# Kernel tuning notes

Measured on AMD Instinct MI355X. Metric: run time of the kernel, lower is better.

Reference implementation:

```python
import jax, jax.numpy as jnp
import numpy as np
from jax import lax

T = 32768
INPUT = 1024
HIDDEN = 1024
OUTPUT = 1024


def setup_inputs() -> dict:
    key = jax.random.key(0)
    k1, k2, k3, k4, k5 = jax.random.split(key, 5)
    return {
        "x": jax.random.normal(k1, (1, T, INPUT), dtype=jnp.float32),
        "W_i2h": jax.random.normal(k2, (HIDDEN, INPUT + HIDDEN), dtype=jnp.float32) * 0.02,
        "b_i2h": jax.random.normal(k3, (HIDDEN,), dtype=jnp.float32) * 0.02,
        "W_h2o": jax.random.normal(k4, (OUTPUT, HIDDEN), dtype=jnp.float32) * 0.02,
        "b_h2o": jax.random.normal(k5, (OUTPUT,), dtype=jnp.float32) * 0.02,
    }


def reference(x, W_i2h, b_i2h, W_h2o, b_h2o):
    # x: [1, T, input]; original iterates timesteps of x[0] with batch-1 state.
    seq = x[0]  # [T, input]
    h0 = jnp.zeros((1, HIDDEN), dtype=x.dtype)

    # Split i2h weight so we avoid a per-step concat: [hidden, input+hidden]
    W_x = W_i2h[:, :INPUT]   # acts on token
    W_h = W_i2h[:, INPUT:]   # acts on hidden

    def step(h, x_t):
        # h: [1, hidden], x_t: [input]
        h_new = jnp.tanh(x_t[None, :] @ W_x.T + h @ W_h.T + b_i2h)
        return h_new, None

    h_T, _ = lax.scan(step, h0, seq)
    # Original computes h2o every step but returns only the last output.
    output = h_T @ W_h2o.T + b_h2o  # [1, output]
    return output
```

## Files before the change

kernel.cpp:

```cpp
#include <hip/hip_runtime.h>

#define T_STEPS 32768
#define HID 1024
#define NWG 64
#define RPG 16

__device__ __forceinline__ unsigned short f2bf(float f) {
    unsigned u = __float_as_uint(f);
    u = (u + 0x7fffu + ((u >> 16) & 1u)) >> 16;
    return (unsigned short)u;
}
__device__ __forceinline__ float bf2f(unsigned short s) {
    return __uint_as_float(((unsigned)s) << 16);
}

#define BM 64
#define BN 64
#define BK 16
#define LDST 68

__global__ void __launch_bounds__(256) pre_gemm(
    const float* __restrict__ x, const float* __restrict__ Wi,
    const float* __restrict__ b, unsigned short* __restrict__ pre)
{
    __shared__ float As[BK * LDST];
    __shared__ float Bs[BK * LDST];
    const int tid = threadIdx.x;
    const int t0 = blockIdx.x * BM;
    const int j0 = blockIdx.y * BN;
    const int row = tid >> 2;
    const int kq  = tid & 3;
    const int tx  = tid & 15;
    const int ty  = tid >> 4;

    float c[4][4];
#pragma unroll
    for (int i = 0; i < 4; ++i)
#pragma unroll
        for (int j = 0; j < 4; ++j) c[i][j] = 0.f;

    for (int k0 = 0; k0 < 1024; k0 += BK) {
        float4 a4 = *(const float4*)&x[(size_t)(t0 + row) * 1024 + k0 + 4 * kq];
        float4 b4 = *(const float4*)&Wi[(size_t)(j0 + row) * 2048 + k0 + 4 * kq];
        __syncthreads();
        As[(4 * kq + 0) * LDST + row] = a4.x;
        As[(4 * kq + 1) * LDST + row] = a4.y;
        As[(4 * kq + 2) * LDST + row] = a4.z;
        As[(4 * kq + 3) * LDST + row] = a4.w;
        Bs[(4 * kq + 0) * LDST + row] = b4.x;
        Bs[(4 * kq + 1) * LDST + row] = b4.y;
        Bs[(4 * kq + 2) * LDST + row] = b4.z;
        Bs[(4 * kq + 3) * LDST + row] = b4.w;
        __syncthreads();
#pragma unroll
        for (int kk = 0; kk < BK; ++kk) {
            float4 av = *(const float4*)&As[kk * LDST + 4 * ty];
            float4 bv = *(const float4*)&Bs[kk * LDST + 4 * tx];
            c[0][0] = fmaf(av.x, bv.x, c[0][0]); c[0][1] = fmaf(av.x, bv.y, c[0][1]);
            c[0][2] = fmaf(av.x, bv.z, c[0][2]); c[0][3] = fmaf(av.x, bv.w, c[0][3]);
            c[1][0] = fmaf(av.y, bv.x, c[1][0]); c[1][1] = fmaf(av.y, bv.y, c[1][1]);
            c[1][2] = fmaf(av.y, bv.z, c[1][2]); c[1][3] = fmaf(av.y, bv.w, c[1][3]);
            c[2][0] = fmaf(av.z, bv.x, c[2][0]); c[2][1] = fmaf(av.z, bv.y, c[2][1]);
            c[2][2] = fmaf(av.z, bv.z, c[2][2]); c[2][3] = fmaf(av.z, bv.w, c[2][3]);
            c[3][0] = fmaf(av.w, bv.x, c[3][0]); c[3][1] = fmaf(av.w, bv.y, c[3][1]);
            c[3][2] = fmaf(av.w, bv.z, c[3][2]); c[3][3] = fmaf(av.w, bv.w, c[3][3]);
        }
    }

    float4 bias = *(const float4*)&b[j0 + 4 * tx];
#pragma unroll
    for (int i = 0; i < 4; ++i) {
        int r = t0 + 4 * ty + i;
        ushort4 u;
        u.x = f2bf(c[i][0] + bias.x);
        u.y = f2bf(c[i][1] + bias.y);
        u.z = f2bf(c[i][2] + bias.z);
        u.w = f2bf(c[i][3] + bias.w);
        *(ushort4*)&pre[(size_t)r * 1024 + j0 + 4 * tx] = u;
    }
}


__device__ __forceinline__ unsigned long long pack_hv(float v, unsigned t) {
    return ((unsigned long long)t << 32) | (unsigned long long)__float_as_uint(v);
}

__device__ __forceinline__ void poll_stage(unsigned long long* src, float* dst,
                                           unsigned tg, int e0)
{
    unsigned long long p0, p1, p2, p3;
    for (;;) {
        p0 = __hip_atomic_load(&src[e0 + 0], __ATOMIC_RELAXED, __HIP_MEMORY_SCOPE_AGENT);
        p1 = __hip_atomic_load(&src[e0 + 1], __ATOMIC_RELAXED, __HIP_MEMORY_SCOPE_AGENT);
        p2 = __hip_atomic_load(&src[e0 + 2], __ATOMIC_RELAXED, __HIP_MEMORY_SCOPE_AGENT);
        p3 = __hip_atomic_load(&src[e0 + 3], __ATOMIC_RELAXED, __HIP_MEMORY_SCOPE_AGENT);
        if ((unsigned)(p0 >> 32) == tg && (unsigned)(p1 >> 32) == tg &&
            (unsigned)(p2 >> 32) == tg && (unsigned)(p3 >> 32) == tg) break;
    }
    dst[e0 + 0] = __uint_as_float((unsigned)p0);
    dst[e0 + 1] = __uint_as_float((unsigned)p1);
    dst[e0 + 2] = __uint_as_float((unsigned)p2);
    dst[e0 + 3] = __uint_as_float((unsigned)p3);
}

__device__ __forceinline__ float wave_sum(float v) {
#pragma unroll
    for (int off = 32; off > 0; off >>= 1) v += __shfl_xor(v, off, 64);
    return v;
}

__global__ void __launch_bounds__(256) rnn_rec(
    const unsigned short* __restrict__ pre,
    const float* __restrict__ Wi,
    const float* __restrict__ Wo,
    const float* __restrict__ bo,
    float* __restrict__ out,
    unsigned long long* hp)
{
    const int g   = blockIdx.x;
    const int tid = threadIdx.x;
    const int w   = tid >> 6;
    const int l   = tid & 63;
    const int rowbase = g * RPG + w * 4;
    const int e0 = tid * 4;

    __shared__ float hl[2][HID];

    float4 wv[4][4];
#pragma unroll
    for (int rr = 0; rr < 4; ++rr)
#pragma unroll
        for (int j = 0; j < 4; ++j)
            wv[rr][j] = *(const float4*)&Wi[(size_t)(rowbase + rr) * 2048 + 1024 + 4 * l + 256 * j];

    if (tid < RPG)
        __hip_atomic_store(&hp[g * RPG + tid], pack_hv(0.f, 0u),
                           __ATOMIC_RELAXED, __HIP_MEMORY_SCOPE_AGENT);

    for (int t = 1; t <= T_STEPS; ++t) {
        float prev = 0.f;
        if (l < 4) prev = bf2f(pre[(size_t)(t - 1) * HID + rowbase + l]);

        unsigned long long* src = &hp[((t - 1) & 1) * HID];
        float* dst = hl[(t - 1) & 1];
        poll_stage(src, dst, (unsigned)(t - 1), e0);
        __syncthreads();

        float s0 = 0.f, s1 = 0.f, s2 = 0.f, s3 = 0.f;
#pragma unroll
        for (int j = 0; j < 4; ++j) {
            float4 hv = *(const float4*)&dst[4 * l + 256 * j];
            s0 = fmaf(wv[0][j].x, hv.x, s0); s0 = fmaf(wv[0][j].y, hv.y, s0);
            s0 = fmaf(wv[0][j].z, hv.z, s0); s0 = fmaf(wv[0][j].w, hv.w, s0);
            s1 = fmaf(wv[1][j].x, hv.x, s1); s1 = fmaf(wv[1][j].y, hv.y, s1);
            s1 = fmaf(wv[1][j].z, hv.z, s1); s1 = fmaf(wv[1][j].w, hv.w, s1);
            s2 = fmaf(wv[2][j].x, hv.x, s2); s2 = fmaf(wv[2][j].y, hv.y, s2);
            s2 = fmaf(wv[2][j].z, hv.z, s2); s2 = fmaf(wv[2][j].w, hv.w, s2);
            s3 = fmaf(wv[3][j].x, hv.x, s3); s3 = fmaf(wv[3][j].y, hv.y, s3);
            s3 = fmaf(wv[3][j].z, hv.z, s3); s3 = fmaf(wv[3][j].w, hv.w, s3);
        }
        s0 = wave_sum(s0); s1 = wave_sum(s1); s2 = wave_sum(s2); s3 = wave_sum(s3);

        if (l < 4) {
            float sv = (l == 0) ? s0 : (l == 1) ? s1 : (l == 2) ? s2 : s3;
            float h = tanhf(prev + sv);
            __hip_atomic_store(&hp[(t & 1) * HID + rowbase + l], pack_hv(h, (unsigned)t),
                               __ATOMIC_RELAXED, __HIP_MEMORY_SCOPE_AGENT);
        }
    }

    {
        unsigned long long* src = &hp[(T_STEPS & 1) * HID];
        float* dst = hl[0];
        poll_stage(src, dst, (unsigned)T_STEPS, e0);
        __syncthreads();

        float s0 = 0.f, s1 = 0.f, s2 = 0.f, s3 = 0.f;
#pragma unroll
        for (int j = 0; j < 4; ++j) {
            float4 hv = *(const float4*)&dst[4 * l + 256 * j];
            float4 w0 = *(const float4*)&Wo[(size_t)(rowbase + 0) * 1024 + 4 * l + 256 * j];
            float4 w1 = *(const float4*)&Wo[(size_t)(rowbase + 1) * 1024 + 4 * l + 256 * j];
            float4 w2 = *(const float4*)&Wo[(size_t)(rowbase + 2) * 1024 + 4 * l + 256 * j];
            float4 w3 = *(const float4*)&Wo[(size_t)(rowbase + 3) * 1024 + 4 * l + 256 * j];
            s0 = fmaf(w0.x, hv.x, s0); s0 = fmaf(w0.y, hv.y, s0);
            s0 = fmaf(w0.z, hv.z, s0); s0 = fmaf(w0.w, hv.w, s0);
            s1 = fmaf(w1.x, hv.x, s1); s1 = fmaf(w1.y, hv.y, s1);
            s1 = fmaf(w1.z, hv.z, s1); s1 = fmaf(w1.w, hv.w, s1);
            s2 = fmaf(w2.x, hv.x, s2); s2 = fmaf(w2.y, hv.y, s2);
            s2 = fmaf(w2.z, hv.z, s2); s2 = fmaf(w2.w, hv.w, s2);
            s3 = fmaf(w3.x, hv.x, s3); s3 = fmaf(w3.y, hv.y, s3);
            s3 = fmaf(w3.z, hv.z, s3); s3 = fmaf(w3.w, hv.w, s3);
        }
        s0 = wave_sum(s0); s1 = wave_sum(s1); s2 = wave_sum(s2); s3 = wave_sum(s3);
        if (l < 4) {
            float sv = (l == 0) ? s0 : (l == 1) ? s1 : (l == 2) ? s2 : s3;
            out[rowbase + l] = sv + bo[rowbase + l];
        }
    }
}

extern "C" void kernel_launch(void* const* d_in, const int* in_sizes, int n_in,
                              void* d_out, int out_size, void* d_ws, size_t ws_size,
                              hipStream_t stream) {
    const float* x     = (const float*)d_in[0];
    const float* W_i2h = (const float*)d_in[1];
    const float* b_i2h = (const float*)d_in[2];
    const float* W_h2o = (const float*)d_in[3];
    const float* b_h2o = (const float*)d_in[4];
    float* out = (float*)d_out;

    unsigned short* pre = (unsigned short*)d_ws;
    unsigned long long* hp =
        (unsigned long long*)((char*)d_ws + (size_t)T_STEPS * HID * sizeof(unsigned short));

    pre_gemm<<<dim3(T_STEPS / BM, HID / BN), 256, 0, stream>>>(x, W_i2h, b_i2h, pre);
    rnn_rec<<<NWG, 256, 0, stream>>>(pre, W_i2h, W_h2o, b_h2o, out, hp);
}
```

Baseline: 57.47 ms.

## Rework recurrent kernel polling, row mapping, staged pre loads and fast tanh

Rewrites the persistent recurrence kernel. Each 16-lane group now owns one hidden row, reduced with a short 4-step shuffle. Hidden-state polling uses inline-asm double-buffered sc1 loads with a spin budget, and stores go out with sc1 as well. Precomputed input projections are prefetched in 64-step chunks into LDS instead of being read from global memory every step, and tanhf is replaced by an exp/rcp approximation. The intent is to cut per-step latency on the cross-workgroup dependency chain. The risks are slightly lower tanh accuracy and a spin budget that can fall through after timing out.

```diff
diff --git a/kernel.cpp b/kernel.cpp
--- a/kernel.cpp
+++ b/kernel.cpp
@@ -4,6 +4,13 @@
 #define HID 1024
 #define NWG 64
 #define RPG 16
+#define PRE_BYTES ((size_t)T_STEPS * HID * 2)
+#define HP_BYTES  (2 * HID * 8)
+
+typedef float vf4 __attribute__((ext_vector_type(4)));
+typedef unsigned uv4 __attribute__((ext_vector_type(4)));
+typedef unsigned uv2 __attribute__((ext_vector_type(2)));
+typedef unsigned long long u64;
 
 __device__ __forceinline__ unsigned short f2bf(float f) {
     unsigned u = __float_as_uint(f);
@@ -80,124 +87,171 @@
     }
 }
 
-
-__device__ __forceinline__ unsigned long long pack_hv(float v, unsigned t) {
-    return ((unsigned long long)t << 32) | (unsigned long long)__float_as_uint(v);
-}
-
-__device__ __forceinline__ void poll_stage(unsigned long long* src, float* dst,
-                                           unsigned tg, int e0)
-{
-    unsigned long long p0, p1, p2, p3;
+__device__ __forceinline__ void st8_sc1(u64* p, u64 v) {
+    asm volatile("global_store_dwordx2 %0, %1, off sc1" :: "v"(p), "v"(v) : "memory");
+}
+__device__ __forceinline__ vf4 ldg4_pin(const float* p) {
+    vf4 r;
+    asm volatile("global_load_dwordx4 %0, %1, off\n\ts_waitcnt vmcnt(0)"
+                 : "=v"(r) : "v"(p) : "memory");
+    return r;
+}
+__device__ __forceinline__ void issue32(uv4& a, uv4& b, const u64* p) {
+    asm volatile("global_load_dwordx4 %0, %2, off sc1\n\t"
+                 "global_load_dwordx4 %1, %2, off offset:16 sc1"
+                 : "=v"(a), "=v"(b) : "v"(p));
+}
+__device__ __forceinline__ void wait2(uv4& a, uv4& b) {
+    asm volatile("s_waitcnt vmcnt(2)" : "+v"(a), "+v"(b));
+}
+__device__ __forceinline__ bool hit4(uv4 a, uv4 b, unsigned tg) {
+    return (a.y == tg) & (a.w == tg) & (b.y == tg) & (b.w == tg);
+}
+__device__ __forceinline__ u64 pack_hv(float v, unsigned t) {
+    return ((u64)t << 32) | (u64)__float_as_uint(v);
+}
+__device__ __forceinline__ float fast_tanh(float x) {
+    float a = fabsf(x);
+    float e = __expf(a + a);
+    float r = 1.f - 2.f * __builtin_amdgcn_rcpf(e + 1.f);
+    return copysignf(r, x);
+}
+
+__device__ __forceinline__ vf4 poll4(const u64* pp, unsigned tg, int& budget) {
+    uv4 a0, b0, a1, b1, ra, rb;
+    issue32(a0, b0, pp);
     for (;;) {
-        p0 = __hip_atomic_load(&src[e0 + 0], __ATOMIC_RELAXED, __HIP_MEMORY_SCOPE_AGENT);
-        p1 = __hip_atomic_load(&src[e0 + 1], __ATOMIC_RELAXED, __HIP_MEMORY_SCOPE_AGENT);
-        p2 = __hip_atomic_load(&src[e0 + 2], __ATOMIC_RELAXED, __HIP_MEMORY_SCOPE_AGENT);
-        p3 = __hip_atomic_load(&src[e0 + 3], __ATOMIC_RELAXED, __HIP_MEMORY_SCOPE_AGENT);
-        if ((unsigned)(p0 >> 32) == tg && (unsigned)(p1 >> 32) == tg &&
-            (unsigned)(p2 >> 32) == tg && (unsigned)(p3 >> 32) == tg) break;
-    }
-    dst[e0 + 0] = __uint_as_float((unsigned)p0);
-    dst[e0 + 1] = __uint_as_float((unsigned)p1);
-    dst[e0 + 2] = __uint_as_float((unsigned)p2);
-    dst[e0 + 3] = __uint_as_float((unsigned)p3);
-}
-
-__device__ __forceinline__ float wave_sum(float v) {
-#pragma unroll
-    for (int off = 32; off > 0; off >>= 1) v += __shfl_xor(v, off, 64);
-    return v;
-}
-
-__global__ void __launch_bounds__(256) rnn_rec(
+        issue32(a1, b1, pp);
+        wait2(a0, b0);
+        if (hit4(a0, b0, tg) || --budget < 0) { ra = a0; rb = b0; break; }
+        issue32(a0, b0, pp);
+        wait2(a1, b1);
+        if (hit4(a1, b1, tg) || --budget < 0) { ra = a1; rb = b1; break; }
+    }
+    asm volatile("s_waitcnt vmcnt(0)"
+                 : "+v"(a0), "+v"(b0), "+v"(a1), "+v"(b1));
+    return (vf4){__uint_as_float(ra.x), __uint_as_float(ra.z),
+                 __uint_as_float(rb.x), __uint_as_float(rb.z)};
+}
+
+__global__ void __launch_bounds__(256, 2) rnn_rec(
     const unsigned short* __restrict__ pre,
     const float* __restrict__ Wi,
     const float* __restrict__ Wo,
     const float* __restrict__ bo,
     float* __restrict__ out,
-    unsigned long long* hp)
+    u64* hp)
 {
-    const int g   = blockIdx.x;
     const int tid = threadIdx.x;
+    const int l   = tid & 63;
     const int w   = tid >> 6;
-    const int l   = tid & 63;
-    const int rowbase = g * RPG + w * 4;
+    const int grp = l >> 4;
+    const int li  = l & 15;
+    const int rows0 = blockIdx.x * RPG;
+    const int myrow = rows0 + 4 * w + grp;
     const int e0 = tid * 4;
 
-    __shared__ float hl[2][HID];
-
-    float4 wv[4][4];
-#pragma unroll
-    for (int rr = 0; rr < 4; ++rr)
-#pragma unroll
-        for (int j = 0; j < 4; ++j)
-            wv[rr][j] = *(const float4*)&Wi[(size_t)(rowbase + rr) * 2048 + 1024 + 4 * l + 256 * j];
-
-    if (tid < RPG)
-        __hip_atomic_store(&hp[g * RPG + tid], pack_hv(0.f, 0u),
-                           __ATOMIC_RELAXED, __HIP_MEMORY_SCOPE_AGENT);
+    __shared__ __align__(16) float hl[2][HID];
+    __shared__ __align__(16) unsigned short stage[2][64][RPG];
+
+    vf4 wv[16];
+    {
+        const float* wp = Wi + (size_t)myrow * 2048 + 1024 + li * 4;
+#pragma unroll
+        for (int j = 0; j < 16; ++j) wv[j] = ldg4_pin(wp + 64 * j);
+    }
+
+    {
+        const int i = tid >> 2, c = (tid & 3) * 4;
+        *(ushort4*)&stage[0][i][c] = *(const ushort4*)&pre[(size_t)i * HID + rows0 + c];
+    }
+    __syncthreads();
+
+    int budget = 4000000;
+    uv2 refv = (uv2){0, 0};
 
     for (int t = 1; t <= T_STEPS; ++t) {
-        float prev = 0.f;
-        if (l < 4) prev = bf2f(pre[(size_t)(t - 1) * HID + rowbase + l]);
-
-        unsigned long long* src = &hp[((t - 1) & 1) * HID];
-        float* dst = hl[(t - 1) & 1];
-        poll_stage(src, dst, (unsigned)(t - 1), e0);
-        __syncthreads();
-
-        float s0 = 0.f, s1 = 0.f, s2 = 0.f, s3 = 0.f;
-#pragma unroll
-        for (int j = 0; j < 4; ++j) {
-            float4 hv = *(const float4*)&dst[4 * l + 256 * j];
-            s0 = fmaf(wv[0][j].x, hv.x, s0); s0 = fmaf(wv[0][j].y, hv.y, s0);
-            s0 = fmaf(wv[0][j].z, hv.z, s0); s0 = fmaf(wv[0][j].w, hv.w, s0);
-            s1 = fmaf(wv[1][j].x, hv.x, s1); s1 = fmaf(wv[1][j].y, hv.y, s1);
-            s1 = fmaf(wv[1][j].z, hv.z, s1); s1 = fmaf(wv[1][j].w, hv.w, s1);
-            s2 = fmaf(wv[2][j].x, hv.x, s2); s2 = fmaf(wv[2][j].y, hv.y, s2);
-            s2 = fmaf(wv[2][j].z, hv.z, s2); s2 = fmaf(wv[2][j].w, hv.w, s2);
-            s3 = fmaf(wv[3][j].x, hv.x, s3); s3 = fmaf(wv[3][j].y, hv.y, s3);
-            s3 = fmaf(wv[3][j].z, hv.z, s3); s3 = fmaf(wv[3][j].w, hv.w, s3);
-        }
-        s0 = wave_sum(s0); s1 = wave_sum(s1); s2 = wave_sum(s2); s3 = wave_sum(s3);
-
-        if (l < 4) {
-            float sv = (l == 0) ? s0 : (l == 1) ? s1 : (l == 2) ? s2 : s3;
-            float h = tanhf(prev + sv);
-            __hip_atomic_store(&hp[(t & 1) * HID + rowbase + l], pack_hv(h, (unsigned)t),
-                               __ATOMIC_RELAXED, __HIP_MEMORY_SCOPE_AGENT);
+        const int par = (t - 1) & 1;
+        const int cb  = (t - 1) >> 6;
+        const int ph  = (t - 1) & 63;
+
+        vf4 hv = poll4(hp + (size_t)par * HID + e0, (unsigned)(t - 1), budget);
+        *(vf4*)&hl[par][e0] = hv;
+
+        if (ph == 40 && cb + 1 < T_STEPS / 64) {
+            asm volatile("s_waitcnt vmcnt(0)" : "+v"(refv));
+            const int i = tid >> 2, c = (tid & 3) * 4;
+            *(uv2*)&stage[(cb + 1) & 1][i][c] = refv;
+        }
+        __syncthreads();
+
+        float prevv = bf2f(stage[cb & 1][ph][4 * w + grp]);
+
+        if (ph == 32 && cb + 1 < T_STEPS / 64) {
+            const int i = tid >> 2, c = (tid & 3) * 4;
+            const unsigned short* q = &pre[(size_t)((cb + 1) * 64 + i) * HID + rows0 + c];
+            asm volatile("global_load_dwordx2 %0, %1, off" : "=v"(refv) : "v"(q));
+        }
+
+        const float* hb = hl[par];
+        float acc0 = 0.f, acc1 = 0.f;
+#pragma unroll
+        for (int j = 0; j < 16; j += 2) {
+            vf4 a = *(const vf4*)&hb[li * 4 + 64 * j];
+            vf4 b = *(const vf4*)&hb[li * 4 + 64 * (j + 1)];
+            acc0 = fmaf(wv[j].x, a.x, acc0);
+            acc0 = fmaf(wv[j].y, a.y, acc0);
+            acc0 = fmaf(wv[j].z, a.z, acc0);
+            acc0 = fmaf(wv[j].w, a.w, acc0);
+            acc1 = fmaf(wv[j + 1].x, b.x, acc1);
+            acc1 = fmaf(wv[j + 1].y, b.y, acc1);
+            acc1 = fmaf(wv[j + 1].z, b.z, acc1);
+            acc1 = fmaf(wv[j + 1].w, b.w, acc1);
+        }
+        float s = acc0 + acc1;
+        s += __shfl_xor(s, 1);
+        s += __shfl_xor(s, 2);
+        s += __shfl_xor(s, 4);
+        s += __shfl_xor(s, 8);
+
+        if (li == 0) {
+            float h = fast_tanh(prevv + s);
+            st8_sc1(&hp[(size_t)(t & 1) * HID + myrow], pack_hv(h, (unsigned)t));
         }
     }
 
     {
-        unsigned long long* src = &hp[(T_STEPS & 1) * HID];
-        float* dst = hl[0];
-        poll_stage(src, dst, (unsigned)T_STEPS, e0);
-        __syncthreads();
-
-        float s0 = 0.f, s1 = 0.f, s2 = 0.f, s3 = 0.f;
-#pragma unroll
-        for (int j = 0; j < 4; ++j) {
-            float4 hv = *(const float4*)&dst[4 * l + 256 * j];
-            float4 w0 = *(const float4*)&Wo[(size_t)(rowbase + 0) * 1024 + 4 * l + 256 * j];
-            float4 w1 = *(const float4*)&Wo[(size_t)(rowbase + 1) * 1024 + 4 * l + 256 * j];
-            float4 w2 = *(const float4*)&Wo[(size_t)(rowbase + 2) * 1024 + 4 * l + 256 * j];
-            float4 w3 = *(const float4*)&Wo[(size_t)(rowbase + 3) * 1024 + 4 * l + 256 * j];
-            s0 = fmaf(w0.x, hv.x, s0); s0 = fmaf(w0.y, hv.y, s0);
-            s0 = fmaf(w0.z, hv.z, s0); s0 = fmaf(w0.w, hv.w, s0);
-            s1 = fmaf(w1.x, hv.x, s1); s1 = fmaf(w1.y, hv.y, s1);
-            s1 = fmaf(w1.z, hv.z, s1); s1 = fmaf(w1.w, hv.w, s1);
-            s2 = fmaf(w2.x, hv.x, s2); s2 = fmaf(w2.y, hv.y, s2);
-            s2 = fmaf(w2.z, hv.z, s2); s2 = fmaf(w2.w, hv.w, s2);
-            s3 = fmaf(w3.x, hv.x, s3); s3 = fmaf(w3.y, hv.y, s3);
-            s3 = fmaf(w3.z, hv.z, s3); s3 = fmaf(w3.w, hv.w, s3);
-        }
-        s0 = wave_sum(s0); s1 = wave_sum(s1); s2 = wave_sum(s2); s3 = wave_sum(s3);
-        if (l < 4) {
-            float sv = (l == 0) ? s0 : (l == 1) ? s1 : (l == 2) ? s2 : s3;
-            out[rowbase + l] = sv + bo[rowbase + l];
-        }
-    }
+        vf4 hv = poll4(hp + (size_t)((T_STEPS & 1) * HID) + e0,
+                       (unsigned)T_STEPS, budget);
+        *(vf4*)&hl[0][e0] = hv;
+        __syncthreads();
+
+        const float* hb = hl[0];
+        const float* wo = Wo + (size_t)myrow * 1024;
+        float acc0 = 0.f, acc1 = 0.f;
+#pragma unroll
+        for (int j = 0; j < 16; j += 2) {
+            vf4 a  = *(const vf4*)&hb[li * 4 + 64 * j];
+            vf4 b  = *(const vf4*)&hb[li * 4 + 64 * (j + 1)];
+            vf4 wa = *(const vf4*)&wo[li * 4 + 64 * j];
+            vf4 wb = *(const vf4*)&wo[li * 4 + 64 * (j + 1)];
+            acc0 = fmaf(wa.x, a.x, acc0);
+            acc0 = fmaf(wa.y, a.y, acc0);
+            acc0 = fmaf(wa.z, a.z, acc0);
+            acc0 = fmaf(wa.w, a.w, acc0);
+            acc1 = fmaf(wb.x, b.x, acc1);
+            acc1 = fmaf(wb.y, b.y, acc1);
+            acc1 = fmaf(wb.z, b.z, acc1);
+            acc1 = fmaf(wb.w, b.w, acc1);
+        }
+        float s = acc0 + acc1;
+        s += __shfl_xor(s, 1);
+        s += __shfl_xor(s, 2);
+        s += __shfl_xor(s, 4);
+        s += __shfl_xor(s, 8);
+        if (li == 0) out[myrow] = s + bo[myrow];
+    }
+    asm volatile("s_waitcnt vmcnt(0)" ::: "memory");
 }
 
 extern "C" void kernel_launch(void* const* d_in, const int* in_sizes, int n_in,
@@ -210,10 +264,11 @@
     const float* b_h2o = (const float*)d_in[4];
     float* out = (float*)d_out;
 
-    unsigned short* pre = (unsigned short*)d_ws;
-    unsigned long long* hp =
-        (unsigned long long*)((char*)d_ws + (size_t)T_STEPS * HID * sizeof(unsigned short));
-
+    char* base = (char*)d_ws;
+    unsigned short* pre = (unsigned short*)base;
+    u64* hp = (u64*)(base + PRE_BYTES);
+
+    hipMemsetAsync(hp, 0, HP_BYTES, stream);
     pre_gemm<<<dim3(T_STEPS / BM, HID / BN), 256, 0, stream>>>(x, W_i2h, b_i2h, pre);
     rnn_rec<<<NWG, 256, 0, stream>>>(pre, W_i2h, W_h2o, b_h2o, out, hp);
 }
```

After: 71.11 ms. +23.7%, slower.
